# Kernel tuning notes

Hardware: AMD Instinct MI355X
Metric: run time of the kernel (lower is better)

Reference implementation:

```python
import jax, jax.numpy as jnp
import numpy as np

B, N, K = 16, 2048, 16          # clouds, points per cloud, knn k
C_IN, C_OUT = 64, 64

def setup_inputs() -> dict:
    key = jax.random.key(0)
    ks = jax.random.split(key, 8)
    s_in = 1.0 / np.sqrt(C_IN)
    return {
        "x": jax.random.normal(ks[0], (B * N, C_IN), jnp.float32),
        "pos": jax.random.normal(ks[1], (B * N, 3), jnp.float32),
        "batch": jnp.repeat(jnp.arange(B, dtype=jnp.int32), N),
        "W_pos": jax.random.normal(ks[2], (3, C_OUT), jnp.float32) / np.sqrt(3.0),
        "b_pos": jnp.zeros((C_OUT,), jnp.float32),
        "W_attn": jax.random.normal(ks[3], (C_OUT, C_OUT), jnp.float32) / np.sqrt(C_OUT),
        "b_attn": jnp.zeros((C_OUT,), jnp.float32),
        "W_val": jax.random.normal(ks[4], (C_IN, C_OUT), jnp.float32) * s_in,
        "W_src": jax.random.normal(ks[5], (C_IN, C_OUT), jnp.float32) * s_in,
        "W_dst": jax.random.normal(ks[6], (C_IN, C_OUT), jnp.float32) * s_in,
    }

def _gather(a, idx):
    # a: [B, N, D], idx: [B, N, K+1] -> [B, N, K+1, D]
    return jax.vmap(lambda ab, ib: ab[ib])(a, idx)

def reference(x, pos, batch, W_pos, b_pos, W_attn, b_attn, W_val, W_src, W_dst):
    # batch is assumed contiguous with equal-size clouds (B clouds of N points),
    # so batch-restricted knn_graph == per-cloud knn after reshape.
    posr = pos.reshape(B, N, 3)
    xr = x.reshape(B, N, C_IN)
    # knn_graph(loop=False): exclude self, then PointTransformerConv re-adds self loops
    d2 = jnp.sum((posr[:, :, None, :] - posr[:, None, :, :]) ** 2, axis=-1)  # [B,N,N]
    d2 = d2 + jnp.eye(N, dtype=d2.dtype) * 1e10
    _, nbr = jax.lax.top_k(-d2, K)                                # [B,N,K] sources j per target i
    self_idx = jnp.broadcast_to(jnp.arange(N)[None, :, None], (B, N, 1))
    nbr = jnp.concatenate([nbr, self_idx], axis=2)                # self loop -> [B,N,K+1]
    alpha_i = xr @ W_dst                                          # lin_dst(x_i)  [B,N,C_OUT]
    alpha_j = _gather(xr @ W_src, nbr)                            # lin_src(x_j)  [B,N,K+1,C_OUT]
    val_j = _gather(xr @ W_val, nbr)                              # lin(x_j)
    pos_j = _gather(posr, nbr)                                    # [B,N,K+1,3]
    delta = (posr[:, :, None, :] - pos_j) @ W_pos + b_pos         # pos_nn(pos_i - pos_j)
    alpha = alpha_i[:, :, None, :] - alpha_j + delta              # subtraction attention
    alpha = alpha @ W_attn + b_attn                               # attn_nn
    alpha = jax.nn.softmax(alpha, axis=2)                         # segment softmax per target i
    out = jnp.sum(alpha * (val_j + delta), axis=2)                # weighted scatter-sum
    return out.reshape(B * N, C_OUT)
```

## Files before the change

kernel.cpp:

```cpp
#include <hip/hip_runtime.h>
#include <math.h>

#define BBATCH 16
#define NPC    2048
#define KNBR   16
#define NPTS   (BBATCH*NPC)

#define NGEMM     128
#define NKNN      2048
#define KNN_WAVES 16
#define BUFCAP    512

__global__ __launch_bounds__(1024) void fused1_kernel(
    const float* __restrict__ pos, const float* __restrict__ x,
    const float* __restrict__ Wpos, const float* __restrict__ bpos,
    const float* __restrict__ Wattn, const float* __restrict__ battn,
    const float* __restrict__ Wval, const float* __restrict__ Wsrc,
    const float* __restrict__ Wdst,
    int* __restrict__ nbr, float* __restrict__ A2, float* __restrict__ S2,
    float* __restrict__ V, float* __restrict__ WP2, float* __restrict__ bb) {
  __shared__ __align__(16) char smem[65536];
  int t = threadIdx.x;
  int bid = blockIdx.x;

  if (bid == 0) {
    if (t < 64) {
      int c = t;
      for (int r = 0; r < 3; ++r) {
        float a = 0.f;
        for (int d = 0; d < 64; ++d) a += Wpos[r * 64 + d] * Wattn[d * 64 + c];
        WP2[r * 64 + c] = a;
      }
      float a = battn[c];
      for (int d = 0; d < 64; ++d) a += bpos[d] * Wattn[d * 64 + c];
      bb[c] = a;
    }
    return;
  }

  if (bid <= NGEMM) {
    int gb = bid - 1;
    float* R0 = (float*)smem;
    float* R1 = (float*)(smem + 16384);
    float* R2 = (float*)(smem + 32768);
    float* R3 = (float*)(smem + 49152);
    float4* R04 = (float4*)R0;
    float4* R34 = (float4*)R3;
    int c = t & 63, g = t >> 6;

    R34[t] = ((const float4*)Wattn)[t];
    R04[t] = ((const float4*)Wdst)[t];
    __syncthreads();
    {
      float a0 = 0, a1 = 0, a2 = 0, a3 = 0;
      for (int k = 0; k < 64; ++k) {
        float w = R3[k * 64 + c];
        a0 += R0[(g * 4 + 0) * 64 + k] * w;
        a1 += R0[(g * 4 + 1) * 64 + k] * w;
        a2 += R0[(g * 4 + 2) * 64 + k] * w;
        a3 += R0[(g * 4 + 3) * 64 + k] * w;
      }
      R1[(g * 4 + 0) * 64 + c] = a0; R1[(g * 4 + 1) * 64 + c] = a1;
      R1[(g * 4 + 2) * 64 + c] = a2; R1[(g * 4 + 3) * 64 + c] = a3;
    }
    __syncthreads();
    R04[t] = ((const float4*)Wsrc)[t];
    __syncthreads();
    {
      float a0 = 0, a1 = 0, a2 = 0, a3 = 0;
      for (int k = 0; k < 64; ++k) {
        float w = R3[k * 64 + c];
        a0 += R0[(g * 4 + 0) * 64 + k] * w;
        a1 += R0[(g * 4 + 1) * 64 + k] * w;
        a2 += R0[(g * 4 + 2) * 64 + k] * w;
        a3 += R0[(g * 4 + 3) * 64 + k] * w;
      }
      R2[(g * 4 + 0) * 64 + c] = a0; R2[(g * 4 + 1) * 64 + c] = a1;
      R2[(g * 4 + 2) * 64 + c] = a2; R2[(g * 4 + 3) * 64 + c] = a3;
    }
    __syncthreads();
    R34[t] = ((const float4*)Wval)[t];
    __syncthreads();

    for (int tile = 0; tile < 4; ++tile) {
      int R = gb * 256 + tile * 64;
      R04[t] = ((const float4*)(x + (size_t)R * 64))[t];
      __syncthreads();
      float v0 = 0, v1 = 0, v2 = 0, v3 = 0;
      float a0 = 0, a1 = 0, a2 = 0, a3 = 0;
      float s0 = 0, s1 = 0, s2 = 0, s3 = 0;
      const float4* xr0 = (const float4*)(R0 + (g * 4 + 0) * 64);
      const float4* xr1 = (const float4*)(R0 + (g * 4 + 1) * 64);
      const float4* xr2 = (const float4*)(R0 + (g * 4 + 2) * 64);
      const float4* xr3 = (const float4*)(R0 + (g * 4 + 3) * 64);
#pragma unroll 4
      for (int k4 = 0; k4 < 16; ++k4) {
        float4 q0 = xr0[k4], q1 = xr1[k4], q2 = xr2[k4], q3 = xr3[k4];
#pragma unroll
        for (int kk = 0; kk < 4; ++kk) {
          int k = k4 * 4 + kk;
          float wv = R3[k * 64 + c];
          float wa = R1[k * 64 + c];
          float ws = R2[k * 64 + c];
          float e0 = (kk == 0) ? q0.x : (kk == 1) ? q0.y : (kk == 2) ? q0.z : q0.w;
          float e1 = (kk == 0) ? q1.x : (kk == 1) ? q1.y : (kk == 2) ? q1.z : q1.w;
          float e2 = (kk == 0) ? q2.x : (kk == 1) ? q2.y : (kk == 2) ? q2.z : q2.w;
          float e3 = (kk == 0) ? q3.x : (kk == 1) ? q3.y : (kk == 2) ? q3.z : q3.w;
          v0 += e0 * wv; v1 += e1 * wv; v2 += e2 * wv; v3 += e3 * wv;
          a0 += e0 * wa; a1 += e1 * wa; a2 += e2 * wa; a3 += e3 * wa;
          s0 += e0 * ws; s1 += e1 * ws; s2 += e2 * ws; s3 += e3 * ws;
        }
      }
      size_t o0 = ((size_t)R + g * 4 + 0) * 64 + c;
      V[o0] = v0; A2[o0] = a0; S2[o0] = s0;
      size_t o1 = o0 + 64;  V[o1] = v1; A2[o1] = a1; S2[o1] = s1;
      size_t o2 = o0 + 128; V[o2] = v2; A2[o2] = a2; S2[o2] = s2;
      size_t o3 = o0 + 192; V[o3] = v3; A2[o3] = a3; S2[o3] = s3;
      __syncthreads();
    }
    return;
  }

  int kb = bid - (NGEMM + 1);
  float4* pos4 = (float4*)smem;
  unsigned short* buf = (unsigned short*)(smem + 32768);
  int* ctr = (int*)(smem + 32768 + 16384);

  int cloud = kb >> 7;
  const float* pc = pos + (size_t)cloud * NPC * 3;
  for (int p = t; p < NPC; p += 1024)
    pos4[p] = make_float4(pc[3 * p], pc[3 * p + 1], pc[3 * p + 2], 0.f);
  int w = t >> 6, lane = t & 63;
  if (lane == 0) ctr[w] = 0;
  __syncthreads();

  int gi = kb * KNN_WAVES + w;
  int ti = gi & (NPC - 1);
  float4 tp = pos4[ti];
  float tx = tp.x, ty = tp.y, tz = tp.z;

  int bkt[32];
#pragma unroll
  for (int c = 0; c < 32; ++c) {
    int j = c * 64 + lane;
    float4 q = pos4[j];
    float dx = tx - q.x, dy = ty - q.y, dz = tz - q.z;
    float d2 = dx * dx + dy * dy + dz * dz;
    int b = (int)(__float_as_uint(d2) >> 20) - 896;
    b = max(0, min(255, b));
    if (j == ti) b = 255;
    bkt[c] = b;
  }

  int lo = 0, hi = 255;
  for (int it = 0; it < 8; ++it) {
    int mid = (lo + hi) >> 1;
    int cnt = 0;
#pragma unroll
    for (int c = 0; c < 32; ++c)
      cnt += (int)__popcll(__ballot(bkt[c] <= mid));
    if (cnt >= 16) hi = mid; else lo = mid + 1;
  }
  int Tp1 = min(hi + 1, 255);

#pragma unroll
  for (int c = 0; c < 32; ++c) {
    if (bkt[c] <= Tp1) {
      int p = atomicAdd(&ctr[w], 1);
      if (p < BUFCAP) buf[w * BUFCAP + p] = (unsigned short)(c * 64 + lane);
    }
  }
  __syncthreads();

  int n = min(ctr[w], BUFCAP);
  double txd = (double)tx, tyd = (double)ty, tzd = (double)tz;

  if (n <= 64) {
    unsigned long long gb = 0xFFFFFFFFFFFFFFFFull;
    int gj = 0x40000000 + lane;
    if (lane < n) {
      int j = buf[w * BUFCAP + lane];
      if (j != ti) {
        float4 q = pos4[j];
        double dx = __dsub_rn(txd, (double)q.x);
        double dy = __dsub_rn(tyd, (double)q.y);
        double dz = __dsub_rn(tzd, (double)q.z);
        double d2 = __dadd_rn(__dadd_rn(__dmul_rn(dx, dx), __dmul_rn(dy, dy)),
                              __dmul_rn(dz, dz));
        gb = (unsigned long long)__double_as_longlong(d2);
        gj = j;
      }
    }
    for (int k = 2; k <= 64; k <<= 1) {
      for (int jj = k >> 1; jj > 0; jj >>= 1) {
        unsigned long long ob = __shfl_xor(gb, jj);
        int oj = __shfl_xor(gj, jj);
        bool keepmin = (((lane & k) == 0) == ((lane & jj) == 0));
        bool less = (ob < gb) || (ob == gb && oj < gj);
        if (keepmin == less) { gb = ob; gj = oj; }
      }
    }
    if (lane < KNBR) nbr[(size_t)gi * KNBR + lane] = gj;
  } else {
    unsigned long long kb2[8];
    int id2[8];
#pragma unroll
    for (int r = 0; r < 8; ++r) {
      int e = r * 64 + lane;
      kb2[r] = 0xFFFFFFFFFFFFFFFFull;
      id2[r] = 0x40000000 + e;
      if (e < n) {
        int j = buf[w * BUFCAP + e];
        if (j != ti) {
          float4 q = pos4[j];
          double dx = __dsub_rn(txd, (double)q.x);
          double dy = __dsub_rn(tyd, (double)q.y);
          double dz = __dsub_rn(tzd, (double)q.z);
          double d2 = __dadd_rn(__dadd_rn(__dmul_rn(dx, dx), __dmul_rn(dy, dy)),
                                __dmul_rn(dz, dz));
          kb2[r] = (unsigned long long)__double_as_longlong(d2);
          id2[r] = j;
        }
      }
    }
    for (int r = 0; r < KNBR; ++r) {
      unsigned long long lb = kb2[0];
      int lj = id2[0];
#pragma unroll
      for (int c = 1; c < 8; ++c)
        if (kb2[c] < lb || (kb2[c] == lb && id2[c] < lj)) {
          lb = kb2[c]; lj = id2[c];
        }
      unsigned long long gb2 = lb;
      int gj2 = lj;
#pragma unroll
      for (int d = 32; d >= 1; d >>= 1) {
        unsigned long long ob = __shfl_xor(gb2, d);
        int oj = __shfl_xor(gj2, d);
        if (ob < gb2 || (ob == gb2 && oj < gj2)) { gb2 = ob; gj2 = oj; }
      }
#pragma unroll
      for (int c = 0; c < 8; ++c)
        if (id2[c] == gj2) kb2[c] = 0xFFFFFFFFFFFFFFFFull;
      if (lane == 0) nbr[(size_t)gi * KNBR + r] = gj2;
    }
  }
}

__global__ __launch_bounds__(256) void edge_kernel(
    const float* __restrict__ pos, const int* __restrict__ nbr,
    const float* __restrict__ A2, const float* __restrict__ S2,
    const float* __restrict__ V, const float* __restrict__ WP2,
    const float* __restrict__ bbv, const float* __restrict__ Wpos,
    const float* __restrict__ bpos, float* __restrict__ out) {
  int t = threadIdx.x, w = t >> 6, c = t & 63;
  int gi = blockIdx.x * 4 + w;
  int cloudbase = gi & ~(NPC - 1);
  float pix = pos[(size_t)gi * 3], piy = pos[(size_t)gi * 3 + 1],
        piz = pos[(size_t)gi * 3 + 2];
  float a2 = A2[(size_t)gi * 64 + c];
  float wp0 = WP2[c], wp1 = WP2[64 + c], wp2 = WP2[128 + c], bbc = bbv[c];
  float u0 = Wpos[c], u1 = Wpos[64 + c], u2 = Wpos[128 + c], bpc = bpos[c];

  float lg[17], vl[17];
#pragma unroll
  for (int e = 0; e < 17; ++e) {
    int j = (e < 16) ? nbr[(size_t)gi * KNBR + e] : (gi & (NPC - 1));
    int jg = cloudbase + j;
    float dx = pix - pos[(size_t)jg * 3];
    float dy = piy - pos[(size_t)jg * 3 + 1];
    float dz = piz - pos[(size_t)jg * 3 + 2];
    float s2 = S2[(size_t)jg * 64 + c];
    float v = V[(size_t)jg * 64 + c];
    lg[e] = a2 - s2 + dx * wp0 + dy * wp1 + dz * wp2 + bbc;
    vl[e] = v + dx * u0 + dy * u1 + dz * u2 + bpc;
  }
  float mx = lg[0];
#pragma unroll
  for (int e = 1; e < 17; ++e) mx = fmaxf(mx, lg[e]);
  float den = 0.f, acc = 0.f;
#pragma unroll
  for (int e = 0; e < 17; ++e) {
    float wgt = __expf(lg[e] - mx);
    den += wgt;
    acc += wgt * vl[e];
  }
  out[(size_t)gi * 64 + c] = acc / den;
}

extern "C" void kernel_launch(void* const* d_in, const int* in_sizes, int n_in,
                              void* d_out, int out_size, void* d_ws, size_t ws_size,
                              hipStream_t stream) {
  const float* x     = (const float*)d_in[0];
  const float* pos   = (const float*)d_in[1];
  const float* Wpos  = (const float*)d_in[3];
  const float* bpos  = (const float*)d_in[4];
  const float* Wattn = (const float*)d_in[5];
  const float* battn = (const float*)d_in[6];
  const float* Wval  = (const float*)d_in[7];
  const float* Wsrc  = (const float*)d_in[8];
  const float* Wdst  = (const float*)d_in[9];

  float* ws  = (float*)d_ws;
  float* A2  = ws;
  float* S2  = A2 + (size_t)NPTS * 64;
  float* V   = S2 + (size_t)NPTS * 64;
  float* WP2 = V + (size_t)NPTS * 64;
  float* bb  = WP2 + 192;
  int*   nbr = (int*)(bb + 64);
  float* out = (float*)d_out;

  fused1_kernel<<<NGEMM + NKNN + 1, 1024, 0, stream>>>(
      pos, x, Wpos, bpos, Wattn, battn, Wval, Wsrc, Wdst,
      nbr, A2, S2, V, WP2, bb);
  edge_kernel<<<NPTS / 4, 256, 0, stream>>>(pos, nbr, A2, S2, V, WP2, bb,
                                            Wpos, bpos, out);
}
```

Baseline: 233.5 us.

## Rebalance fused GEMM/kNN blocks and amortize per-cloud position loads

Rebalances the fused kernel's work split. It now launches 512 GEMM blocks of 64 rows each instead of 128 blocks of 256 rows, and 512 kNN blocks where each wave handles four targets instead of one, so each block's load of a cloud's positions into shared memory is reused over 64 targets. The shared-memory atomic buffer append is replaced by a ballot/mbcnt prefix compaction. The self point is no longer forced into the last bucket; instead the threshold search requires 17 candidates, and self is still excluded later by index. The setup block moves to the last block index. In exchange, each GEMM block now recomputes the folded attention weights for only 64 rows, which increases redundant prologue work.

```diff
diff --git a/kernel.cpp b/kernel.cpp
--- a/kernel.cpp
+++ b/kernel.cpp
@@ -5,13 +5,11 @@
 #define NPC    2048
 #define KNBR   16
 #define NPTS   (BBATCH*NPC)
-
-#define NGEMM     128
-#define NKNN      2048
-#define KNN_WAVES 16
-#define BUFCAP    512
-
-__global__ __launch_bounds__(1024) void fused1_kernel(
+#define NGEMM  512
+#define NKNN   512
+#define BUFCAP 512
+
+__global__ __launch_bounds__(1024) void fused_gk_kernel(
     const float* __restrict__ pos, const float* __restrict__ x,
     const float* __restrict__ Wpos, const float* __restrict__ bpos,
     const float* __restrict__ Wattn, const float* __restrict__ battn,
@@ -22,31 +20,29 @@
   __shared__ __align__(16) char smem[65536];
   int t = threadIdx.x;
   int bid = blockIdx.x;
-
-  if (bid == 0) {
+  int c = t & 63, g = t >> 6;
+
+  if (bid == NGEMM + NKNN) {
     if (t < 64) {
-      int c = t;
       for (int r = 0; r < 3; ++r) {
         float a = 0.f;
-        for (int d = 0; d < 64; ++d) a += Wpos[r * 64 + d] * Wattn[d * 64 + c];
-        WP2[r * 64 + c] = a;
-      }
-      float a = battn[c];
-      for (int d = 0; d < 64; ++d) a += bpos[d] * Wattn[d * 64 + c];
-      bb[c] = a;
+        for (int d = 0; d < 64; ++d) a += Wpos[r * 64 + d] * Wattn[d * 64 + t];
+        WP2[r * 64 + t] = a;
+      }
+      float a = battn[t];
+      for (int d = 0; d < 64; ++d) a += bpos[d] * Wattn[d * 64 + t];
+      bb[t] = a;
     }
     return;
   }
 
-  if (bid <= NGEMM) {
-    int gb = bid - 1;
+  if (bid < NGEMM) {
     float* R0 = (float*)smem;
     float* R1 = (float*)(smem + 16384);
     float* R2 = (float*)(smem + 32768);
     float* R3 = (float*)(smem + 49152);
     float4* R04 = (float4*)R0;
     float4* R34 = (float4*)R3;
-    int c = t & 63, g = t >> 6;
 
     R34[t] = ((const float4*)Wattn)[t];
     R04[t] = ((const float4*)Wdst)[t];
@@ -80,137 +76,102 @@
     }
     __syncthreads();
     R34[t] = ((const float4*)Wval)[t];
-    __syncthreads();
-
-    for (int tile = 0; tile < 4; ++tile) {
-      int R = gb * 256 + tile * 64;
-      R04[t] = ((const float4*)(x + (size_t)R * 64))[t];
-      __syncthreads();
-      float v0 = 0, v1 = 0, v2 = 0, v3 = 0;
-      float a0 = 0, a1 = 0, a2 = 0, a3 = 0;
-      float s0 = 0, s1 = 0, s2 = 0, s3 = 0;
-      const float4* xr0 = (const float4*)(R0 + (g * 4 + 0) * 64);
-      const float4* xr1 = (const float4*)(R0 + (g * 4 + 1) * 64);
-      const float4* xr2 = (const float4*)(R0 + (g * 4 + 2) * 64);
-      const float4* xr3 = (const float4*)(R0 + (g * 4 + 3) * 64);
+    R04[t] = ((const float4*)(x + (size_t)bid * 64 * 64))[t];
+    __syncthreads();
+
+    float v0 = 0, v1 = 0, v2 = 0, v3 = 0;
+    float a0 = 0, a1 = 0, a2 = 0, a3 = 0;
+    float s0 = 0, s1 = 0, s2 = 0, s3 = 0;
+    const float4* xr0 = (const float4*)(R0 + (g * 4 + 0) * 64);
+    const float4* xr1 = (const float4*)(R0 + (g * 4 + 1) * 64);
+    const float4* xr2 = (const float4*)(R0 + (g * 4 + 2) * 64);
+    const float4* xr3 = (const float4*)(R0 + (g * 4 + 3) * 64);
 #pragma unroll 4
-      for (int k4 = 0; k4 < 16; ++k4) {
-        float4 q0 = xr0[k4], q1 = xr1[k4], q2 = xr2[k4], q3 = xr3[k4];
-#pragma unroll
-        for (int kk = 0; kk < 4; ++kk) {
-          int k = k4 * 4 + kk;
-          float wv = R3[k * 64 + c];
-          float wa = R1[k * 64 + c];
-          float ws = R2[k * 64 + c];
-          float e0 = (kk == 0) ? q0.x : (kk == 1) ? q0.y : (kk == 2) ? q0.z : q0.w;
-          float e1 = (kk == 0) ? q1.x : (kk == 1) ? q1.y : (kk == 2) ? q1.z : q1.w;
-          float e2 = (kk == 0) ? q2.x : (kk == 1) ? q2.y : (kk == 2) ? q2.z : q2.w;
-          float e3 = (kk == 0) ? q3.x : (kk == 1) ? q3.y : (kk == 2) ? q3.z : q3.w;
-          v0 += e0 * wv; v1 += e1 * wv; v2 += e2 * wv; v3 += e3 * wv;
-          a0 += e0 * wa; a1 += e1 * wa; a2 += e2 * wa; a3 += e3 * wa;
-          s0 += e0 * ws; s1 += e1 * ws; s2 += e2 * ws; s3 += e3 * ws;
-        }
-      }
-      size_t o0 = ((size_t)R + g * 4 + 0) * 64 + c;
-      V[o0] = v0; A2[o0] = a0; S2[o0] = s0;
-      size_t o1 = o0 + 64;  V[o1] = v1; A2[o1] = a1; S2[o1] = s1;
-      size_t o2 = o0 + 128; V[o2] = v2; A2[o2] = a2; S2[o2] = s2;
-      size_t o3 = o0 + 192; V[o3] = v3; A2[o3] = a3; S2[o3] = s3;
-      __syncthreads();
-    }
+    for (int k4 = 0; k4 < 16; ++k4) {
+      float4 q0 = xr0[k4], q1 = xr1[k4], q2 = xr2[k4], q3 = xr3[k4];
+#pragma unroll
+      for (int kk = 0; kk < 4; ++kk) {
+        int k = k4 * 4 + kk;
+        float wv = R3[k * 64 + c];
+        float wa = R1[k * 64 + c];
+        float ws = R2[k * 64 + c];
+        float e0 = (kk == 0) ? q0.x : (kk == 1) ? q0.y : (kk == 2) ? q0.z : q0.w;
+        float e1 = (kk == 0) ? q1.x : (kk == 1) ? q1.y : (kk == 2) ? q1.z : q1.w;
+        float e2 = (kk == 0) ? q2.x : (kk == 1) ? q2.y : (kk == 2) ? q2.z : q2.w;
+        float e3 = (kk == 0) ? q3.x : (kk == 1) ? q3.y : (kk == 2) ? q3.z : q3.w;
+        v0 += e0 * wv; v1 += e1 * wv; v2 += e2 * wv; v3 += e3 * wv;
+        a0 += e0 * wa; a1 += e1 * wa; a2 += e2 * wa; a3 += e3 * wa;
+        s0 += e0 * ws; s1 += e1 * ws; s2 += e2 * ws; s3 += e3 * ws;
+      }
+    }
+    size_t o0 = ((size_t)bid * 64 + g * 4 + 0) * 64 + c;
+    V[o0] = v0; A2[o0] = a0; S2[o0] = s0;
+    size_t o1 = o0 + 64;  V[o1] = v1; A2[o1] = a1; S2[o1] = s1;
+    size_t o2 = o0 + 128; V[o2] = v2; A2[o2] = a2; S2[o2] = s2;
+    size_t o3 = o0 + 192; V[o3] = v3; A2[o3] = a3; S2[o3] = s3;
     return;
   }
 
-  int kb = bid - (NGEMM + 1);
+  int kb = bid - NGEMM;
   float4* pos4 = (float4*)smem;
   unsigned short* buf = (unsigned short*)(smem + 32768);
-  int* ctr = (int*)(smem + 32768 + 16384);
-
-  int cloud = kb >> 7;
+  int cloud = kb >> 5;
   const float* pc = pos + (size_t)cloud * NPC * 3;
   for (int p = t; p < NPC; p += 1024)
     pos4[p] = make_float4(pc[3 * p], pc[3 * p + 1], pc[3 * p + 2], 0.f);
-  int w = t >> 6, lane = t & 63;
-  if (lane == 0) ctr[w] = 0;
   __syncthreads();
 
-  int gi = kb * KNN_WAVES + w;
-  int ti = gi & (NPC - 1);
-  float4 tp = pos4[ti];
-  float tx = tp.x, ty = tp.y, tz = tp.z;
-
-  int bkt[32];
-#pragma unroll
-  for (int c = 0; c < 32; ++c) {
-    int j = c * 64 + lane;
-    float4 q = pos4[j];
-    float dx = tx - q.x, dy = ty - q.y, dz = tz - q.z;
-    float d2 = dx * dx + dy * dy + dz * dz;
-    int b = (int)(__float_as_uint(d2) >> 20) - 896;
-    b = max(0, min(255, b));
-    if (j == ti) b = 255;
-    bkt[c] = b;
-  }
-
-  int lo = 0, hi = 255;
-  for (int it = 0; it < 8; ++it) {
-    int mid = (lo + hi) >> 1;
-    int cnt = 0;
-#pragma unroll
-    for (int c = 0; c < 32; ++c)
-      cnt += (int)__popcll(__ballot(bkt[c] <= mid));
-    if (cnt >= 16) hi = mid; else lo = mid + 1;
-  }
-  int Tp1 = min(hi + 1, 255);
-
-#pragma unroll
-  for (int c = 0; c < 32; ++c) {
-    if (bkt[c] <= Tp1) {
-      int p = atomicAdd(&ctr[w], 1);
-      if (p < BUFCAP) buf[w * BUFCAP + p] = (unsigned short)(c * 64 + lane);
-    }
-  }
-  __syncthreads();
-
-  int n = min(ctr[w], BUFCAP);
-  double txd = (double)tx, tyd = (double)ty, tzd = (double)tz;
-
-  if (n <= 64) {
-    unsigned long long gb = 0xFFFFFFFFFFFFFFFFull;
-    int gj = 0x40000000 + lane;
-    if (lane < n) {
-      int j = buf[w * BUFCAP + lane];
-      if (j != ti) {
-        float4 q = pos4[j];
-        double dx = __dsub_rn(txd, (double)q.x);
-        double dy = __dsub_rn(tyd, (double)q.y);
-        double dz = __dsub_rn(tzd, (double)q.z);
-        double d2 = __dadd_rn(__dadd_rn(__dmul_rn(dx, dx), __dmul_rn(dy, dy)),
-                              __dmul_rn(dz, dz));
-        gb = (unsigned long long)__double_as_longlong(d2);
-        gj = j;
-      }
-    }
-    for (int k = 2; k <= 64; k <<= 1) {
-      for (int jj = k >> 1; jj > 0; jj >>= 1) {
-        unsigned long long ob = __shfl_xor(gb, jj);
-        int oj = __shfl_xor(gj, jj);
-        bool keepmin = (((lane & k) == 0) == ((lane & jj) == 0));
-        bool less = (ob < gb) || (ob == gb && oj < gj);
-        if (keepmin == less) { gb = ob; gj = oj; }
-      }
-    }
-    if (lane < KNBR) nbr[(size_t)gi * KNBR + lane] = gj;
-  } else {
-    unsigned long long kb2[8];
-    int id2[8];
-#pragma unroll
-    for (int r = 0; r < 8; ++r) {
-      int e = r * 64 + lane;
-      kb2[r] = 0xFFFFFFFFFFFFFFFFull;
-      id2[r] = 0x40000000 + e;
-      if (e < n) {
-        int j = buf[w * BUFCAP + e];
+  int w = g, lane = c;
+  for (int u = 0; u < 4; ++u) {
+    int lt = u * 16 + w;
+    int gi = kb * 64 + lt;
+    int ti = gi & (NPC - 1);
+    float4 tp = pos4[ti];
+    float tx = tp.x, ty = tp.y, tz = tp.z;
+
+    int bkt[32];
+#pragma unroll
+    for (int cc = 0; cc < 32; ++cc) {
+      int j = cc * 64 + lane;
+      float4 q = pos4[j];
+      float dx = tx - q.x, dy = ty - q.y, dz = tz - q.z;
+      float d2 = dx * dx + dy * dy + dz * dz;
+      int b = (int)(__float_as_uint(d2) >> 20) - 896;
+      bkt[cc] = max(0, min(255, b));
+    }
+
+    int lo = 0, hi = 255;
+    for (int it = 0; it < 8; ++it) {
+      int mid = (lo + hi) >> 1;
+      int cnt = 0;
+#pragma unroll
+      for (int cc = 0; cc < 32; ++cc)
+        cnt += (int)__popcll(__ballot(bkt[cc] <= mid));
+      if (cnt >= 17) hi = mid; else lo = mid + 1;
+    }
+    int Tp1 = min(hi + 1, 255);
+
+    int base = 0;
+#pragma unroll
+    for (int cc = 0; cc < 32; ++cc) {
+      bool f = (bkt[cc] <= Tp1);
+      unsigned long long mm = __ballot(f);
+      unsigned int pre = __builtin_amdgcn_mbcnt_hi(
+          (unsigned)(mm >> 32), __builtin_amdgcn_mbcnt_lo((unsigned)mm, 0u));
+      if (f) {
+        int p = base + (int)pre;
+        if (p < BUFCAP) buf[w * BUFCAP + p] = (unsigned short)(cc * 64 + lane);
+      }
+      base += (int)__popcll(mm);
+    }
+    int n = min(base, BUFCAP);
+    double txd = (double)tx, tyd = (double)ty, tzd = (double)tz;
+
+    if (n <= 64) {
+      unsigned long long gb = 0xFFFFFFFFFFFFFFFFull;
+      int gj = 0x40000000 + lane;
+      if (lane < n) {
+        int j = buf[w * BUFCAP + lane];
         if (j != ti) {
           float4 q = pos4[j];
           double dx = __dsub_rn(txd, (double)q.x);
@@ -218,31 +179,64 @@
           double dz = __dsub_rn(tzd, (double)q.z);
           double d2 = __dadd_rn(__dadd_rn(__dmul_rn(dx, dx), __dmul_rn(dy, dy)),
                                 __dmul_rn(dz, dz));
-          kb2[r] = (unsigned long long)__double_as_longlong(d2);
-          id2[r] = j;
+          gb = (unsigned long long)__double_as_longlong(d2);
+          gj = j;
         }
       }
-    }
-    for (int r = 0; r < KNBR; ++r) {
-      unsigned long long lb = kb2[0];
-      int lj = id2[0];
-#pragma unroll
-      for (int c = 1; c < 8; ++c)
-        if (kb2[c] < lb || (kb2[c] == lb && id2[c] < lj)) {
-          lb = kb2[c]; lj = id2[c];
+      for (int k = 2; k <= 64; k <<= 1) {
+        for (int jj = k >> 1; jj > 0; jj >>= 1) {
+          unsigned long long ob = __shfl_xor(gb, jj);
+          int oj = __shfl_xor(gj, jj);
+          bool keepmin = (((lane & k) == 0) == ((lane & jj) == 0));
+          bool less = (ob < gb) || (ob == gb && oj < gj);
+          if (keepmin == less) { gb = ob; gj = oj; }
         }
-      unsigned long long gb2 = lb;
-      int gj2 = lj;
-#pragma unroll
-      for (int d = 32; d >= 1; d >>= 1) {
-        unsigned long long ob = __shfl_xor(gb2, d);
-        int oj = __shfl_xor(gj2, d);
-        if (ob < gb2 || (ob == gb2 && oj < gj2)) { gb2 = ob; gj2 = oj; }
-      }
-#pragma unroll
-      for (int c = 0; c < 8; ++c)
-        if (id2[c] == gj2) kb2[c] = 0xFFFFFFFFFFFFFFFFull;
-      if (lane == 0) nbr[(size_t)gi * KNBR + r] = gj2;
+      }
+      if (lane < KNBR) nbr[(size_t)gi * KNBR + lane] = gj;
+    } else {
+      unsigned long long kb2[8];
+      int id2[8];
+#pragma unroll
+      for (int r = 0; r < 8; ++r) {
+        int e = r * 64 + lane;
+        kb2[r] = 0xFFFFFFFFFFFFFFFFull;
+        id2[r] = 0x40000000 + e;
+        if (e < n) {
+          int j = buf[w * BUFCAP + e];
+          if (j != ti) {
+            float4 q = pos4[j];
+            double dx = __dsub_rn(txd, (double)q.x);
+            double dy = __dsub_rn(tyd, (double)q.y);
+            double dz = __dsub_rn(tzd, (double)q.z);
+            double d2 = __dadd_rn(
+                __dadd_rn(__dmul_rn(dx, dx), __dmul_rn(dy, dy)),
+                __dmul_rn(dz, dz));
+            kb2[r] = (unsigned long long)__double_as_longlong(d2);
+            id2[r] = j;
+          }
+        }
+      }
+      for (int r = 0; r < KNBR; ++r) {
+        unsigned long long lb = kb2[0];
+        int lj = id2[0];
+#pragma unroll
+        for (int cc = 1; cc < 8; ++cc)
+          if (kb2[cc] < lb || (kb2[cc] == lb && id2[cc] < lj)) {
+            lb = kb2[cc]; lj = id2[cc];
+          }
+        unsigned long long gb2 = lb;
+        int gj2 = lj;
+#pragma unroll
+        for (int d = 32; d >= 1; d >>= 1) {
+          unsigned long long ob = __shfl_xor(gb2, d);
+          int oj = __shfl_xor(gj2, d);
+          if (ob < gb2 || (ob == gb2 && oj < gj2)) { gb2 = ob; gj2 = oj; }
+        }
+#pragma unroll
+        for (int cc = 0; cc < 8; ++cc)
+          if (id2[cc] == gj2) kb2[cc] = 0xFFFFFFFFFFFFFFFFull;
+        if (lane == 0) nbr[(size_t)gi * KNBR + r] = gj2;
+      }
     }
   }
 }
@@ -310,7 +304,7 @@
   int*   nbr = (int*)(bb + 64);
   float* out = (float*)d_out;
 
-  fused1_kernel<<<NGEMM + NKNN + 1, 1024, 0, stream>>>(
+  fused_gk_kernel<<<NGEMM + NKNN + 1, 1024, 0, stream>>>(
       pos, x, Wpos, bpos, Wattn, battn, Wval, Wsrc, Wdst,
       nbr, A2, S2, V, WP2, bb);
   edge_kernel<<<NPTS / 4, 256, 0, stream>>>(pos, nbr, A2, S2, V, WP2, bb,
```

Result: faster. 224.0 us (-4.1%).
